# Optimization experiments

Measured on AMD Instinct MI355X. Metric: run time of the kernel, lower is better.

Reference implementation:

```python
import jax, jax.numpy as jnp
import numpy as np

V, C, L, NH, NKV, HID, E, K, T, B = 32000, 1536, 2, 12, 4, 2048, 8, 2, 2048, 1
D = C // NH  # 128
NREP = NH // NKV
EPS = 1e-6

def _rms(x, w):
    return x * jax.lax.rsqrt(jnp.mean(x * x, axis=-1, keepdims=True) + EPS) * w


def setup_inputs() -> dict:
    key = jax.random.key(0)
    ks = jax.random.split(key, 14)
    s = 0.02
    inp = {
        "tokens": jax.random.randint(ks[0], (B, T), 0, V, dtype=jnp.int64),
        "emb": jax.random.normal(ks[1], (V, C), jnp.float32) * s,      # tied with output proj
        "pos": jax.random.normal(ks[2], (T, C), jnp.float32) * s,
        "wq": jax.random.normal(ks[3], (L, C, NH * D), jnp.float32) * s,
        "wk": jax.random.normal(ks[4], (L, C, NKV * D), jnp.float32) * s,
        "wv": jax.random.normal(ks[5], (L, C, NKV * D), jnp.float32) * s,
        "wo": jax.random.normal(ks[6], (L, C, C), jnp.float32) * s,
        "attn_norm_w": jnp.ones((L, C), jnp.float32),
        "ffn_norm_w": jnp.ones((L, C), jnp.float32),
        "gate": jax.random.normal(ks[7], (L, C, E), jnp.float32) * s,
        "ew1": jax.random.normal(ks[8], (L, E, C, HID), jnp.float32) * s,
        "ew2": jax.random.normal(ks[9], (L, E, HID, C), jnp.float32) * s,
        "ew3": jax.random.normal(ks[10], (L, E, C, HID), jnp.float32) * s,
        "final_norm_w": jnp.ones((C,), jnp.float32),
    }
    return inp


def _forward(tokens, emb, pos, wq, wk, wv, wo, attn_norm_w, ffn_norm_w, gate,
             ew1, ew2, ew3, final_norm_w):
    x = emb[tokens] + pos[None, :T]            # [B,T,C]; dropout=0 (eval)
    causal = jnp.tril(jnp.ones((T, T), bool))
    for l in range(L):
        # --- GQA attention ---
        h = _rms(x, attn_norm_w[l])
        q = (h @ wq[l]).reshape(B, T, NH, D).transpose(0, 2, 1, 3)     # [B,NH,T,D]
        k = (h @ wk[l]).reshape(B, T, NKV, D).transpose(0, 2, 1, 3)
        v = (h @ wv[l]).reshape(B, T, NKV, D).transpose(0, 2, 1, 3)
        k = jnp.repeat(k, NREP, axis=1)
        v = jnp.repeat(v, NREP, axis=1)
        scores = jnp.einsum("bhqd,bhkd->bhqk", q, k) / jnp.sqrt(jnp.float32(D))
        scores = jnp.where(causal, scores, jnp.finfo(scores.dtype).min)
        attn = jax.nn.softmax(scores, axis=-1)
        y = jnp.einsum("bhqk,bhkd->bhqd", attn, v)
        y = y.transpose(0, 2, 1, 3).reshape(B, T, C)
        x = x + y @ wo[l]
        # --- MoE FFN (top-k routed SwiGLU experts) ---
        xf = _rms(x, ffn_norm_w[l]).reshape(-1, C)                      # [N,C]
        probs = jax.nn.softmax(xf @ gate[l], axis=-1)                   # [N,E]
        topw, topi = jax.lax.top_k(probs, K)
        topw = topw / jnp.sum(topw, axis=-1, keepdims=True)
        dense_w = jnp.sum(jax.nn.one_hot(topi, E, dtype=xf.dtype) * topw[..., None], axis=1)  # [N,E]
        h1 = jnp.einsum("nc,ech->enh", xf, ew1[l])
        h3 = jnp.einsum("nc,ech->enh", xf, ew3[l])
        hh = jax.nn.silu(h1) * h3                                       # [E,N,HID]
        moe = jnp.einsum("ne,enh,ehc->nc", dense_w, hh, ew2[l])
        x = x + moe.reshape(B, T, C)
    x = _rms(x, final_norm_w)
    logits = x @ emb.T                                                   # tied output proj
    return logits


def reference(tokens, emb, pos, wq, wk, wv, wo, attn_norm_w, ffn_norm_w, gate,
              ew1, ew2, ew3, final_norm_w):
    return _forward(tokens, emb, pos, wq, wk, wv, wo, attn_norm_w, ffn_norm_w,
                    gate, ew1, ew2, ew3, final_norm_w)
```

## Files before the change

kernel.cpp:

```cpp
#include <hip/hip_runtime.h>
#include <hip/hip_bf16.h>
#include <math.h>

#define Tn   2048
#define Cn   1536
#define Vn   32000
#define NHn  12
#define NKVn 4
#define Dn   128
#define HIDn 2048
#define En   8
#define Kn   2
#define Ln   2
#define NREPn 3
#define EPSn 1e-6f

using bf16 = __hip_bfloat16;
using bf16x8 = __attribute__((ext_vector_type(8))) short;
using f32x4v = __attribute__((ext_vector_type(4))) float;

__device__ __forceinline__ void split3(float v, short& h, short& m, short& lo) {
  bf16 b0 = __float2bfloat16(v);
  float r1 = v - __bfloat162float(b0);
  bf16 b1 = __float2bfloat16(r1);
  float r2 = r1 - __bfloat162float(b1);
  bf16 b2 = __float2bfloat16(r2);
  h = *reinterpret_cast<short*>(&b0);
  m = *reinterpret_cast<short*>(&b1);
  lo = *reinterpret_cast<short*>(&b2);
}
__device__ __forceinline__ float b2f(short s) {
  bf16 b = *reinterpret_cast<bf16*>(&s);
  return __bfloat162float(b);
}
__device__ __forceinline__ void gl_lds16(const void* g, void* l) {
  __builtin_amdgcn_global_load_lds((const __attribute__((address_space(1))) void*)g,
                                   (__attribute__((address_space(3))) void*)l, 16, 0, 0);
}

__global__ void embed_k(const int* __restrict__ tok, const float* __restrict__ emb,
                        const float* __restrict__ pos, float* __restrict__ x) {
  int n = blockIdx.x;
  int t = threadIdx.x;
  int id = tok[n];
  const float* er = emb + (size_t)id * Cn;
  const float* pr = pos + (size_t)n * Cn;
  float* xr = x + (size_t)n * Cn;
  for (int c = t; c < Cn; c += 256) xr[c] = er[c] + pr[c];
}

__global__ void rmsnorm_k(const float* __restrict__ x, const float* __restrict__ w,
                          float* __restrict__ out) {
  int n = blockIdx.x, t = threadIdx.x;
  const float* xr = x + (size_t)n * Cn;
  float v[6];
  float ss = 0.f;
#pragma unroll
  for (int i = 0; i < 6; i++) { v[i] = xr[t + i * 256]; ss += v[i] * v[i]; }
  for (int off = 32; off > 0; off >>= 1) ss += __shfl_down(ss, off, 64);
  __shared__ float red[4];
  __shared__ float rtot;
  int wave = t >> 6, lane = t & 63;
  if (lane == 0) red[wave] = ss;
  __syncthreads();
  if (t == 0) rtot = rsqrtf((red[0] + red[1] + red[2] + red[3]) / (float)Cn + EPSn);
  __syncthreads();
  float r = rtot;
  float* orow = out + (size_t)n * Cn;
#pragma unroll
  for (int i = 0; i < 6; i++) { int c = t + i * 256; orow[c] = v[i] * r * w[c]; }
}

__global__ void f2b_k(const float* __restrict__ s, bf16* __restrict__ d, size_t n4) {
  size_t i = (size_t)blockIdx.x * 256 + threadIdx.x;
  size_t stride = (size_t)gridDim.x * 256;
  for (; i < n4; i += stride) {
    float4 v = ((const float4*)s)[i];
    d[i * 4 + 0] = __float2bfloat16(v.x);
    d[i * 4 + 1] = __float2bfloat16(v.y);
    d[i * 4 + 2] = __float2bfloat16(v.z);
    d[i * 4 + 3] = __float2bfloat16(v.w);
  }
}

__global__ void splita_k(const float* __restrict__ s, short* __restrict__ dh,
                         short* __restrict__ dm, short* __restrict__ dl, size_t n4) {
  size_t i = (size_t)blockIdx.x * 256 + threadIdx.x;
  size_t stride = (size_t)gridDim.x * 256;
  for (; i < n4; i += stride) {
    float4 v = ((const float4*)s)[i];
    float a[4] = {v.x, v.y, v.z, v.w};
#pragma unroll
    for (int u = 0; u < 4; u++) {
      short h, m, lo;
      split3(a[u], h, m, lo);
      dh[i * 4 + u] = h; dm[i * 4 + u] = m; dl[i * 4 + u] = lo;
    }
  }
}

__global__ void transp3_k(const float* __restrict__ src, short* __restrict__ dh,
                          short* __restrict__ dm, short* __restrict__ dl, int K, int N) {
  __shared__ __align__(16) float ls[32][33];
  size_t boff = (size_t)blockIdx.z * K * N;
  int k0 = blockIdx.x * 32, n0 = blockIdx.y * 32;
  int t = threadIdx.x;
  int kr = t >> 3, n4 = (t & 7) * 4;
  float4 vv = *(const float4*)&src[boff + (size_t)(k0 + kr) * N + n0 + n4];
  ls[kr][n4 + 0] = vv.x; ls[kr][n4 + 1] = vv.y; ls[kr][n4 + 2] = vv.z; ls[kr][n4 + 3] = vv.w;
  __syncthreads();
  int nr = t >> 3, k4 = (t & 7) * 4;
  size_t dbase = boff + (size_t)(n0 + nr) * K + k0 + k4;
#pragma unroll
  for (int u = 0; u < 4; u++) {
    short h, m, lo;
    split3(ls[k4 + u][nr], h, m, lo);
    dh[dbase + u] = h; dm[dbase + u] = m; dl[dbase + u] = lo;
  }
}

__global__ void transp_k(const float* __restrict__ src, bf16* __restrict__ dst, int K, int N) {
  __shared__ __align__(16) float ls[32][33];
  size_t boff = (size_t)blockIdx.z * K * N;
  int k0 = blockIdx.x * 32, n0 = blockIdx.y * 32;
  int t = threadIdx.x;
  int kr = t >> 3, n4 = (t & 7) * 4;
  float4 vv = *(const float4*)&src[boff + (size_t)(k0 + kr) * N + n0 + n4];
  ls[kr][n4 + 0] = vv.x; ls[kr][n4 + 1] = vv.y; ls[kr][n4 + 2] = vv.z; ls[kr][n4 + 3] = vv.w;
  __syncthreads();
  int nr = t >> 3, k4 = (t & 7) * 4;
  bf16* drow = dst + boff + (size_t)(n0 + nr) * K + k0 + k4;
#pragma unroll
  for (int u = 0; u < 4; u++) drow[u] = __float2bfloat16(ls[k4 + u][nr]);
}

__global__ void __launch_bounds__(256) gemm_btl(const bf16* __restrict__ A, const bf16* __restrict__ Bt,
                                                const float* res, float* Co, int M, int N, int K) {
  __shared__ __align__(16) bf16 As[128 * 32];
  __shared__ __align__(16) bf16 Bs[128 * 32];
  int t = threadIdx.x;
  int l = t & 63, w = t >> 6;
  int bm = blockIdx.x * 128, bn = blockIdx.y * 128;
  int wr = (w >> 1) * 64, wc = (w & 1) * 64;
  const f32x4v zero = {0.f, 0.f, 0.f, 0.f};
  f32x4v acc[4][4];
#pragma unroll
  for (int i = 0; i < 4; i++)
#pragma unroll
    for (int j = 0; j < 4; j++) acc[i][j] = zero;
  const bf16* ag0 = A + (size_t)(bm + (t >> 2)) * K + (t & 3) * 8;
  const bf16* ag1 = A + (size_t)(bm + 64 + (t >> 2)) * K + (t & 3) * 8;
  const bf16* bg0 = Bt + (size_t)(bn + (t >> 2)) * K + (t & 3) * 8;
  const bf16* bg1 = Bt + (size_t)(bn + 64 + (t >> 2)) * K + (t & 3) * 8;
  int rl = l & 15, ko = (l >> 4) * 8;
  for (int k0 = 0; k0 < K; k0 += 32) {
    gl_lds16(ag0 + k0, (char*)As + t * 16);
    gl_lds16(ag1 + k0, (char*)As + (256 + t) * 16);
    gl_lds16(bg0 + k0, (char*)Bs + t * 16);
    gl_lds16(bg1 + k0, (char*)Bs + (256 + t) * 16);
    __syncthreads();
    bf16x8 a[4], b[4];
#pragma unroll
    for (int i = 0; i < 4; i++) a[i] = *(const bf16x8*)(As + (wr + i * 16 + rl) * 32 + ko);
#pragma unroll
    for (int j = 0; j < 4; j++) b[j] = *(const bf16x8*)(Bs + (wc + j * 16 + rl) * 32 + ko);
#pragma unroll
    for (int i = 0; i < 4; i++)
#pragma unroll
      for (int j = 0; j < 4; j++)
        acc[i][j] = __builtin_amdgcn_mfma_f32_16x16x32_bf16(a[i], b[j], acc[i][j], 0, 0, 0);
    __syncthreads();
  }
#pragma unroll
  for (int i = 0; i < 4; i++) {
    int rbase = bm + wr + i * 16 + (l >> 4) * 4;
#pragma unroll
    for (int j = 0; j < 4; j++) {
      int col = bn + wc + j * 16 + (l & 15);
#pragma unroll
      for (int r = 0; r < 4; r++) {
        size_t idx = (size_t)(rbase + r) * N + col;
        float v = acc[i][j][r];
        if (res) v += res[idx];
        Co[idx] = v;
      }
    }
  }
}

__global__ void __launch_bounds__(256) gemm6(const bf16* __restrict__ AH, const bf16* __restrict__ AM,
                                             const bf16* __restrict__ AL,
                                             const bf16* __restrict__ BH, const bf16* __restrict__ BM,
                                             const bf16* __restrict__ BL,
                                             const float* res, float* __restrict__ Co,
                                             int M, int N, int K) {
  __shared__ __align__(16) bf16 sAH[128 * 32], sAM[128 * 32], sAL[128 * 32];
  __shared__ __align__(16) bf16 sBH[128 * 32], sBM[128 * 32], sBL[128 * 32];
  int t = threadIdx.x;
  int l = t & 63, w = t >> 6;
  int bm = blockIdx.x * 128, bn = blockIdx.y * 128;
  int wr = (w >> 1) * 64, wc = (w & 1) * 64;
  const f32x4v zero = {0.f, 0.f, 0.f, 0.f};
  f32x4v acc[4][4];
#pragma unroll
  for (int i = 0; i < 4; i++)
#pragma unroll
    for (int j = 0; j < 4; j++) acc[i][j] = zero;
  size_t a0 = (size_t)(bm + (t >> 2)) * K + (t & 3) * 8;
  size_t a1 = (size_t)(bm + 64 + (t >> 2)) * K + (t & 3) * 8;
  size_t b0 = (size_t)(bn + (t >> 2)) * K + (t & 3) * 8;
  size_t b1 = (size_t)(bn + 64 + (t >> 2)) * K + (t & 3) * 8;
  int rl = l & 15, ko = (l >> 4) * 8;
  for (int k0 = 0; k0 < K; k0 += 32) {
    gl_lds16(AH + a0 + k0, (char*)sAH + t * 16);
    gl_lds16(AH + a1 + k0, (char*)sAH + (256 + t) * 16);
    gl_lds16(AM + a0 + k0, (char*)sAM + t * 16);
    gl_lds16(AM + a1 + k0, (char*)sAM + (256 + t) * 16);
    gl_lds16(AL + a0 + k0, (char*)sAL + t * 16);
    gl_lds16(AL + a1 + k0, (char*)sAL + (256 + t) * 16);
    gl_lds16(BH + b0 + k0, (char*)sBH + t * 16);
    gl_lds16(BH + b1 + k0, (char*)sBH + (256 + t) * 16);
    gl_lds16(BM + b0 + k0, (char*)sBM + t * 16);
    gl_lds16(BM + b1 + k0, (char*)sBM + (256 + t) * 16);
    gl_lds16(BL + b0 + k0, (char*)sBL + t * 16);
    gl_lds16(BL + b1 + k0, (char*)sBL + (256 + t) * 16);
    __syncthreads();
    bf16x8 aH[4], aM[4], aL[4];
#pragma unroll
    for (int i = 0; i < 4; i++) {
      int ro = (wr + i * 16 + rl) * 32 + ko;
      aH[i] = *(const bf16x8*)(sAH + ro);
      aM[i] = *(const bf16x8*)(sAM + ro);
      aL[i] = *(const bf16x8*)(sAL + ro);
    }
#pragma unroll
    for (int j = 0; j < 4; j++) {
      int ro = (wc + j * 16 + rl) * 32 + ko;
      bf16x8 bh = *(const bf16x8*)(sBH + ro);
      bf16x8 bm_ = *(const bf16x8*)(sBM + ro);
      bf16x8 bl = *(const bf16x8*)(sBL + ro);
#pragma unroll
      for (int i = 0; i < 4; i++) {
        acc[i][j] = __builtin_amdgcn_mfma_f32_16x16x32_bf16(aL[i], bh, acc[i][j], 0, 0, 0);
        acc[i][j] = __builtin_amdgcn_mfma_f32_16x16x32_bf16(aH[i], bl, acc[i][j], 0, 0, 0);
        acc[i][j] = __builtin_amdgcn_mfma_f32_16x16x32_bf16(aM[i], bm_, acc[i][j], 0, 0, 0);
        acc[i][j] = __builtin_amdgcn_mfma_f32_16x16x32_bf16(aM[i], bh, acc[i][j], 0, 0, 0);
        acc[i][j] = __builtin_amdgcn_mfma_f32_16x16x32_bf16(aH[i], bm_, acc[i][j], 0, 0, 0);
        acc[i][j] = __builtin_amdgcn_mfma_f32_16x16x32_bf16(aH[i], bh, acc[i][j], 0, 0, 0);
      }
    }
    __syncthreads();
  }
#pragma unroll
  for (int i = 0; i < 4; i++) {
    int rbase = bm + wr + i * 16 + (l >> 4) * 4;
#pragma unroll
    for (int j = 0; j < 4; j++) {
      int col = bn + wc + j * 16 + (l & 15);
#pragma unroll
      for (int r = 0; r < 4; r++) {
        size_t idx = (size_t)(rbase + r) * N + col;
        float v = acc[i][j][r];
        if (res) v += res[idx];
        Co[idx] = v;
      }
    }
  }
}

__global__ void __launch_bounds__(256) mexp6(const bf16* __restrict__ AH, const bf16* __restrict__ AM,
                                             const bf16* __restrict__ AL,
                                             const bf16* __restrict__ BH, const bf16* __restrict__ BM,
                                             const bf16* __restrict__ BL,
                                             const int* __restrict__ perm, const int* __restrict__ cnt,
                                             int ebase,
                                             short* __restrict__ HH, short* __restrict__ HM,
                                             short* __restrict__ HL,
                                             float* __restrict__ Co, int K, int N, int mode) {
  int e = ebase + blockIdx.z;
  int nrows = cnt[e];
  int bm = blockIdx.x * 128;
  if (bm >= nrows) return;
  int bn = blockIdx.y * 128;
  size_t eoff = (size_t)blockIdx.z * K * N;
  __shared__ __align__(16) bf16 sAH[128 * 32], sAM[128 * 32], sAL[128 * 32];
  __shared__ __align__(16) bf16 sBH[128 * 32], sBM[128 * 32], sBL[128 * 32];
  __shared__ int prow[128];
  int t = threadIdx.x, l = t & 63, w = t >> 6;
  if (t < 128) {
    int i = bm + t;
    prow[t] = (i < nrows) ? perm[e * Tn + i] : -1;
  }
  __syncthreads();
  int wr = (w >> 1) * 64, wc = (w & 1) * 64;
  const f32x4v zero = {0.f, 0.f, 0.f, 0.f};
  f32x4v acc[4][4];
#pragma unroll
  for (int i = 0; i < 4; i++)
#pragma unroll
    for (int j = 0; j < 4; j++) acc[i][j] = zero;
  int p0 = prow[t >> 2], p1 = prow[64 + (t >> 2)];
  int g0r = (p0 >= 0) ? (mode == 2 ? p0 : (p0 >> 1)) : 0;
  int g1r = (p1 >= 0) ? (mode == 2 ? p1 : (p1 >> 1)) : 0;
  size_t a0 = (size_t)g0r * K + (t & 3) * 8;
  size_t a1 = (size_t)g1r * K + (t & 3) * 8;
  size_t b0 = eoff + (size_t)(bn + (t >> 2)) * K + (t & 3) * 8;
  size_t b1 = eoff + (size_t)(bn + 64 + (t >> 2)) * K + (t & 3) * 8;
  int rl = l & 15, ko = (l >> 4) * 8;
  for (int k0 = 0; k0 < K; k0 += 32) {
    gl_lds16(AH + a0 + k0, (char*)sAH + t * 16);
    gl_lds16(AH + a1 + k0, (char*)sAH + (256 + t) * 16);
    gl_lds16(AM + a0 + k0, (char*)sAM + t * 16);
    gl_lds16(AM + a1 + k0, (char*)sAM + (256 + t) * 16);
    gl_lds16(AL + a0 + k0, (char*)sAL + t * 16);
    gl_lds16(AL + a1 + k0, (char*)sAL + (256 + t) * 16);
    gl_lds16(BH + b0 + k0, (char*)sBH + t * 16);
    gl_lds16(BH + b1 + k0, (char*)sBH + (256 + t) * 16);
    gl_lds16(BM + b0 + k0, (char*)sBM + t * 16);
    gl_lds16(BM + b1 + k0, (char*)sBM + (256 + t) * 16);
    gl_lds16(BL + b0 + k0, (char*)sBL + t * 16);
    gl_lds16(BL + b1 + k0, (char*)sBL + (256 + t) * 16);
    __syncthreads();
    bf16x8 aH[4], aM[4], aL[4];
#pragma unroll
    for (int i = 0; i < 4; i++) {
      int ro = (wr + i * 16 + rl) * 32 + ko;
      aH[i] = *(const bf16x8*)(sAH + ro);
      aM[i] = *(const bf16x8*)(sAM + ro);
      aL[i] = *(const bf16x8*)(sAL + ro);
    }
#pragma unroll
    for (int j = 0; j < 4; j++) {
      int ro = (wc + j * 16 + rl) * 32 + ko;
      bf16x8 bh = *(const bf16x8*)(sBH + ro);
      bf16x8 bm_ = *(const bf16x8*)(sBM + ro);
      bf16x8 bl = *(const bf16x8*)(sBL + ro);
#pragma unroll
      for (int i = 0; i < 4; i++) {
        acc[i][j] = __builtin_amdgcn_mfma_f32_16x16x32_bf16(aL[i], bh, acc[i][j], 0, 0, 0);
        acc[i][j] = __builtin_amdgcn_mfma_f32_16x16x32_bf16(aH[i], bl, acc[i][j], 0, 0, 0);
        acc[i][j] = __builtin_amdgcn_mfma_f32_16x16x32_bf16(aM[i], bm_, acc[i][j], 0, 0, 0);
        acc[i][j] = __builtin_amdgcn_mfma_f32_16x16x32_bf16(aM[i], bh, acc[i][j], 0, 0, 0);
        acc[i][j] = __builtin_amdgcn_mfma_f32_16x16x32_bf16(aH[i], bm_, acc[i][j], 0, 0, 0);
        acc[i][j] = __builtin_amdgcn_mfma_f32_16x16x32_bf16(aH[i], bh, acc[i][j], 0, 0, 0);
      }
    }
    __syncthreads();
  }
#pragma unroll
  for (int i = 0; i < 4; i++) {
#pragma unroll
    for (int r = 0; r < 4; r++) {
      int lrow = wr + i * 16 + (l >> 4) * 4 + r;
      int p = prow[lrow];
      if (p < 0) continue;
#pragma unroll
      for (int j = 0; j < 4; j++) {
        int col = bn + wc + j * 16 + (l & 15);
        size_t idx = (size_t)p * N + col;
        float v = acc[i][j][r];
        if (mode == 0) {
          short h, m, lo;
          split3(v, h, m, lo);
          HH[idx] = h; HM[idx] = m; HL[idx] = lo;
        } else if (mode == 1) {
          float v1 = b2f(HH[idx]) + b2f(HM[idx]) + b2f(HL[idx]);
          float hh = (v1 / (1.f + expf(-v1))) * v;
          short h, m, lo;
          split3(hh, h, m, lo);
          HH[idx] = h; HM[idx] = m; HL[idx] = lo;
        } else {
          Co[idx] = v;
        }
      }
    }
  }
}

__global__ void __launch_bounds__(256) mexpB(const bf16* __restrict__ A, const bf16* __restrict__ B,
                                             const int* __restrict__ perm, const int* __restrict__ cnt,
                                             int ebase, bf16* __restrict__ HB,
                                             float* __restrict__ Co, int K, int N, int mode) {
  int e = ebase + blockIdx.z;
  int nrows = cnt[e];
  int bm = blockIdx.x * 128;
  if (bm >= nrows) return;
  int bn = blockIdx.y * 128;
  size_t eoff = (size_t)blockIdx.z * K * N;
  __shared__ __align__(16) bf16 sA[128 * 32];
  __shared__ __align__(16) bf16 sB[128 * 32];
  __shared__ int prow[128];
  int t = threadIdx.x, l = t & 63, w = t >> 6;
  if (t < 128) {
    int i = bm + t;
    prow[t] = (i < nrows) ? perm[e * Tn + i] : -1;
  }
  __syncthreads();
  int wr = (w >> 1) * 64, wc = (w & 1) * 64;
  const f32x4v zero = {0.f, 0.f, 0.f, 0.f};
  f32x4v acc[4][4];
#pragma unroll
  for (int i = 0; i < 4; i++)
#pragma unroll
    for (int j = 0; j < 4; j++) acc[i][j] = zero;
  int p0 = prow[t >> 2], p1 = prow[64 + (t >> 2)];
  int g0r = (p0 >= 0) ? (mode == 2 ? p0 : (p0 >> 1)) : 0;
  int g1r = (p1 >= 0) ? (mode == 2 ? p1 : (p1 >> 1)) : 0;
  size_t a0 = (size_t)g0r * K + (t & 3) * 8;
  size_t a1 = (size_t)g1r * K + (t & 3) * 8;
  size_t b0 = eoff + (size_t)(bn + (t >> 2)) * K + (t & 3) * 8;
  size_t b1 = eoff + (size_t)(bn + 64 + (t >> 2)) * K + (t & 3) * 8;
  int rl = l & 15, ko = (l >> 4) * 8;
  for (int k0 = 0; k0 < K; k0 += 32) {
    gl_lds16(A + a0 + k0, (char*)sA + t * 16);
    gl_lds16(A + a1 + k0, (char*)sA + (256 + t) * 16);
    gl_lds16(B + b0 + k0, (char*)sB + t * 16);
    gl_lds16(B + b1 + k0, (char*)sB + (256 + t) * 16);
    __syncthreads();
    bf16x8 a[4], b[4];
#pragma unroll
    for (int i = 0; i < 4; i++) a[i] = *(const bf16x8*)(sA + (wr + i * 16 + rl) * 32 + ko);
#pragma unroll
    for (int j = 0; j < 4; j++) b[j] = *(const bf16x8*)(sB + (wc + j * 16 + rl) * 32 + ko);
#pragma unroll
    for (int i = 0; i < 4; i++)
#pragma unroll
      for (int j = 0; j < 4; j++)
        acc[i][j] = __builtin_amdgcn_mfma_f32_16x16x32_bf16(a[i], b[j], acc[i][j], 0, 0, 0);
    __syncthreads();
  }
#pragma unroll
  for (int i = 0; i < 4; i++) {
#pragma unroll
    for (int r = 0; r < 4; r++) {
      int lrow = wr + i * 16 + (l >> 4) * 4 + r;
      int p = prow[lrow];
      if (p < 0) continue;
#pragma unroll
      for (int j = 0; j < 4; j++) {
        int col = bn + wc + j * 16 + (l & 15);
        size_t idx = (size_t)p * N + col;
        float v = acc[i][j][r];
        if (mode == 0) {
          HB[idx] = __float2bfloat16(v);
        } else if (mode == 1) {
          float v1 = __bfloat162float(HB[idx]);
          HB[idx] = __float2bfloat16((v1 / (1.f + expf(-v1))) * v);
        } else {
          Co[idx] = v;
        }
      }
    }
  }
}

__global__ void __launch_bounds__(256) attn_fast_k(const float* __restrict__ q,
                                                   const float* __restrict__ k,
                                                   const float* __restrict__ v,
                                                   float* __restrict__ y) {
  int qt = gridDim.x - 1 - blockIdx.x;
  int head = blockIdx.y;
  int kvh = head / NREPn;
  int q0 = qt * 32;
  int t = threadIdx.x;
  int r = t >> 3, g = t & 7, d0 = g * 16;
  __shared__ __align__(16) float ks[32][Dn + 4];
  __shared__ __align__(16) float vs[32][Dn + 4];
  const float scale = 0.08838834764831845f;
  float qr[16];
  {
    const float* qrow = q + (size_t)(q0 + r) * (NHn * Dn) + head * Dn + d0;
#pragma unroll
    for (int j = 0; j < 16; j += 4) {
      float4 u = *(const float4*)(qrow + j);
      qr[j] = u.x * scale; qr[j + 1] = u.y * scale;
      qr[j + 2] = u.z * scale; qr[j + 3] = u.w * scale;
    }
  }
  float o[16];
#pragma unroll
  for (int j = 0; j < 16; j++) o[j] = 0.f;
  float rowm = -1e30f, rowl = 0.f;

  for (int kt = 0; kt <= qt; kt++) {
    int kv0 = kt * 32;
    for (int e = t; e < 32 * 32; e += 256) {
      int rr = e >> 5, c4 = (e & 31) * 4;
      size_t off = (size_t)(kv0 + rr) * (NKVn * Dn) + kvh * Dn + c4;
      *(float4*)&ks[rr][c4] = *(const float4*)(k + off);
      *(float4*)&vs[rr][c4] = *(const float4*)(v + off);
    }
    __syncthreads();
    float s[32];
#pragma unroll
    for (int kk = 0; kk < 32; kk++) {
      const float* krow = &ks[kk][d0];
      float p = 0.f;
#pragma unroll
      for (int j = 0; j < 16; j += 4) {
        float4 u = *(const float4*)(krow + j);
        p += qr[j] * u.x + qr[j + 1] * u.y + qr[j + 2] * u.z + qr[j + 3] * u.w;
      }
      p += __shfl_xor(p, 1);
      p += __shfl_xor(p, 2);
      p += __shfl_xor(p, 4);
      s[kk] = p;
    }
    if (kt == qt) {
#pragma unroll
      for (int kk = 0; kk < 32; kk++)
        if (kk > r) s[kk] = -1e30f;
    }
    float mx = s[0];
#pragma unroll
    for (int kk = 1; kk < 32; kk++) mx = fmaxf(mx, s[kk]);
    float m_new = fmaxf(rowm, mx);
    float corr = expf(rowm - m_new);
    float sum = 0.f;
#pragma unroll
    for (int kk = 0; kk < 32; kk++) { s[kk] = expf(s[kk] - m_new); sum += s[kk]; }
    rowl = rowl * corr + sum;
    rowm = m_new;
#pragma unroll
    for (int j = 0; j < 16; j++) o[j] *= corr;
#pragma unroll
    for (int kk = 0; kk < 32; kk++) {
      float p = s[kk];
      const float* vrow = &vs[kk][d0];
#pragma unroll
      for (int j = 0; j < 16; j += 4) {
        float4 u = *(const float4*)(vrow + j);
        o[j] += p * u.x; o[j + 1] += p * u.y; o[j + 2] += p * u.z; o[j + 3] += p * u.w;
      }
    }
    __syncthreads();
  }
  float inv = 1.f / rowl;
  float* yrow = y + (size_t)(q0 + r) * (NHn * Dn) + head * Dn + d0;
#pragma unroll
  for (int j = 0; j < 16; j += 4) {
    float4 u;
    u.x = o[j] * inv; u.y = o[j + 1] * inv; u.z = o[j + 2] * inv; u.w = o[j + 3] * inv;
    *(float4*)(yrow + j) = u;
  }
}

__global__ void gate_k(const float* __restrict__ xf, const float* __restrict__ g,
                       float* __restrict__ gl) {
  int n = blockIdx.x, t = threadIdx.x;
  int e = t & 7, cs = t >> 3;
  const float* xr = xf + (size_t)n * Cn;
  float s = 0.f;
  for (int j = 0; j < Cn / 32; j++) {
    int c = cs + 32 * j;
    s += xr[c] * g[c * En + e];
  }
  __shared__ float red[256];
  red[t] = s;
  __syncthreads();
  if (t < 8) {
    float tot = 0.f;
    for (int j = 0; j < 32; j++) tot += red[t + 8 * j];
    gl[n * En + t] = tot;
  }
}

__global__ void route_k(const float* __restrict__ gl, float* __restrict__ topw,
                        int* __restrict__ cnt, int* __restrict__ perm) {
  int n = blockIdx.x * blockDim.x + threadIdx.x;
  if (n >= Tn) return;
  float p[En];
  float mx = -1e30f;
#pragma unroll
  for (int e = 0; e < En; e++) { p[e] = gl[n * En + e]; mx = fmaxf(mx, p[e]); }
  float s = 0.f;
#pragma unroll
  for (int e = 0; e < En; e++) { p[e] = expf(p[e] - mx); s += p[e]; }
  float invs = 1.f / s;
#pragma unroll
  for (int e = 0; e < En; e++) p[e] *= invs;
  int i0 = 0;
#pragma unroll
  for (int e = 1; e < En; e++) if (p[e] > p[i0]) i0 = e;
  int i1 = (i0 == 0) ? 1 : 0;
#pragma unroll
  for (int e = 0; e < En; e++) if (e != i0 && p[e] > p[i1]) i1 = e;
  float w0 = p[i0], w1 = p[i1], sw = w0 + w1;
  topw[2 * n]     = w0 / sw;
  topw[2 * n + 1] = w1 / sw;
  int pos0 = atomicAdd(&cnt[i0], 1);
  perm[i0 * Tn + pos0] = 2 * n;
  int pos1 = atomicAdd(&cnt[i1], 1);
  perm[i1 * Tn + pos1] = 2 * n + 1;
}

__global__ void combine_k(const float* __restrict__ pairout, const float* __restrict__ topw,
                          float* __restrict__ x) {
  int n = blockIdx.x, t = threadIdx.x;
  float w0 = topw[2 * n], w1 = topw[2 * n + 1];
  const float* p0 = pairout + (size_t)(2 * n) * Cn;
  const float* p1 = pairout + (size_t)(2 * n + 1) * Cn;
  float* xr = x + (size_t)n * Cn;
  for (int c = t; c < Cn; c += 256) xr[c] += w0 * p0[c] + w1 * p1[c];
}

extern "C" void kernel_launch(void* const* d_in, const int* in_sizes, int n_in,
                              void* d_out, int out_size, void* d_ws, size_t ws_size,
                              hipStream_t stream) {
  const int*   tokens = (const int*)d_in[0];
  const float* emb    = (const float*)d_in[1];
  const float* pos    = (const float*)d_in[2];
  const float* wq     = (const float*)d_in[3];
  const float* wk     = (const float*)d_in[4];
  const float* wv     = (const float*)d_in[5];
  const float* wo     = (const float*)d_in[6];
  const float* attn_nw= (const float*)d_in[7];
  const float* ffn_nw = (const float*)d_in[8];
  const float* gate   = (const float*)d_in[9];
  const float* ew1    = (const float*)d_in[10];
  const float* ew2    = (const float*)d_in[11];
  const float* ew3    = (const float*)d_in[12];
  const float* final_nw = (const float*)d_in[13];
  float* out = (float*)d_out;

  char* wsb = (char*)d_ws;
  const size_t NC = (size_t)Tn * Cn;
  size_t off = 0;
  auto alloc = [&](size_t bytes) -> size_t {
    off = (off + 255) & ~(size_t)255;
    size_t p = off;
    off += bytes;
    return p;
  };
  size_t o_x    = alloc(NC * 4);
  size_t o_h    = alloc(NC * 4);
  size_t o_gl   = alloc((size_t)Tn * En * 4);
  size_t o_topw = alloc((size_t)Tn * Kn * 4);
  size_t o_cnt  = alloc(64);
  size_t o_perm = alloc((size_t)En * Tn * 4);
  size_t wlvl   = (size_t)4 * Cn * HIDn * 2;
  size_t o_w    = alloc(3 * wlvl);
  size_t hs_lvl = NC * 2;
  size_t o_hs   = alloc(3 * hs_lvl);
  size_t o_qb   = alloc(NC * 4);
  size_t o_kb   = alloc((size_t)Tn * NKVn * Dn * 4);
  size_t o_vb   = alloc((size_t)Tn * NKVn * Dn * 4);
  size_t o_yb   = alloc(NC * 4);
  size_t hb_lvl = (size_t)Tn * Kn * HIDn * 2;
  size_t o_hbs  = o_qb;
  size_t end_hbs = o_hbs + 3 * hb_lvl;
  if (off < end_hbs) off = end_hbs;
  size_t o_pair = alloc(NC * 4);

  float* x       = (float*)(wsb + o_x);
  float* h       = (float*)(wsb + o_h);
  float* gl      = (float*)(wsb + o_gl);
  float* topw    = (float*)(wsb + o_topw);
  int*   cnt     = (int*)(wsb + o_cnt);
  int*   perm    = (int*)(wsb + o_perm);
  float* qb      = (float*)(wsb + o_qb);
  float* kb      = (float*)(wsb + o_kb);
  float* vb      = (float*)(wsb + o_vb);
  float* yb      = (float*)(wsb + o_yb);
  float* pairout = (float*)(wsb + o_pair);
  bf16*  hb      = (bf16*)(wsb + o_pair);
  bf16*  embB    = (bf16*)(wsb + o_w);

  short* hs[3]; short* hbs[3]; short* ewT[3];
  for (int s = 0; s < 3; s++) {
    hs[s]  = (short*)(wsb + o_hs + (size_t)s * hs_lvl);
    hbs[s] = (short*)(wsb + o_hbs + (size_t)s * hb_lvl);
    ewT[s] = (short*)(wsb + o_w + (size_t)s * wlvl);
  }
  size_t wq_lvl = (size_t)Cn * (NHn * Dn) * 2;
  size_t wk_lvl = (size_t)Cn * (NKVn * Dn) * 2;
  short* wqT[3]; short* wkT[3]; short* wvT[3]; short* woT[3];
  {
    size_t p = o_w;
    for (int s = 0; s < 3; s++) { wqT[s] = (short*)(wsb + p); p += wq_lvl; }
    for (int s = 0; s < 3; s++) { wkT[s] = (short*)(wsb + p); p += wk_lvl; }
    for (int s = 0; s < 3; s++) { wvT[s] = (short*)(wsb + p); p += wk_lvl; }
    for (int s = 0; s < 3; s++) { woT[s] = (short*)(wsb + p); p += wq_lvl; }
  }

  embed_k<<<Tn, 256, 0, stream>>>(tokens, emb, pos, x);
  for (int l = 0; l < Ln; l++) {
    const float* wq_l = wq + (size_t)l * Cn * (NHn * Dn);
    const float* wk_l = wk + (size_t)l * Cn * (NKVn * Dn);
    const float* wv_l = wv + (size_t)l * Cn * (NKVn * Dn);
    const float* wo_l = wo + (size_t)l * Cn * Cn;
    const float* g_l  = gate + (size_t)l * Cn * En;
    const float* e1_l = ew1 + (size_t)l * En * Cn * HIDn;
    const float* e2_l = ew2 + (size_t)l * En * HIDn * Cn;
    const float* e3_l = ew3 + (size_t)l * En * Cn * HIDn;

    transp3_k<<<dim3(Cn / 32, (NHn * Dn) / 32, 1), 256, 0, stream>>>(wq_l, wqT[0], wqT[1], wqT[2], Cn, NHn * Dn);
    transp3_k<<<dim3(Cn / 32, (NKVn * Dn) / 32, 1), 256, 0, stream>>>(wk_l, wkT[0], wkT[1], wkT[2], Cn, NKVn * Dn);
    transp3_k<<<dim3(Cn / 32, (NKVn * Dn) / 32, 1), 256, 0, stream>>>(wv_l, wvT[0], wvT[1], wvT[2], Cn, NKVn * Dn);
    transp3_k<<<dim3(Cn / 32, Cn / 32, 1), 256, 0, stream>>>(wo_l, woT[0], woT[1], woT[2], Cn, Cn);
    rmsnorm_k<<<Tn, 256, 0, stream>>>(x, attn_nw + (size_t)l * Cn, h);
    splita_k<<<2048, 256, 0, stream>>>(h, hs[0], hs[1], hs[2], NC / 4);
    gemm6<<<dim3(Tn / 128, (NHn * Dn) / 128), 256, 0, stream>>>(
        (bf16*)hs[0], (bf16*)hs[1], (bf16*)hs[2], (bf16*)wqT[0], (bf16*)wqT[1], (bf16*)wqT[2],
        nullptr, qb, Tn, NHn * Dn, Cn);
    gemm6<<<dim3(Tn / 128, (NKVn * Dn) / 128), 256, 0, stream>>>(
        (bf16*)hs[0], (bf16*)hs[1], (bf16*)hs[2], (bf16*)wkT[0], (bf16*)wkT[1], (bf16*)wkT[2],
        nullptr, kb, Tn, NKVn * Dn, Cn);
    gemm6<<<dim3(Tn / 128, (NKVn * Dn) / 128), 256, 0, stream>>>(
        (bf16*)hs[0], (bf16*)hs[1], (bf16*)hs[2], (bf16*)wvT[0], (bf16*)wvT[1], (bf16*)wvT[2],
        nullptr, vb, Tn, NKVn * Dn, Cn);
    attn_fast_k<<<dim3(Tn / 32, NHn), 256, 0, stream>>>(qb, kb, vb, yb);
    splita_k<<<2048, 256, 0, stream>>>(yb, hs[0], hs[1], hs[2], NC / 4);
    gemm6<<<dim3(Tn / 128, Cn / 128), 256, 0, stream>>>(
        (bf16*)hs[0], (bf16*)hs[1], (bf16*)hs[2], (bf16*)woT[0], (bf16*)woT[1], (bf16*)woT[2],
        x, x, Tn, Cn, Cn);

    rmsnorm_k<<<Tn, 256, 0, stream>>>(x, ffn_nw + (size_t)l * Cn, h);
    gate_k<<<Tn, 256, 0, stream>>>(h, g_l, gl);
    hipMemsetAsync(cnt, 0, 64, stream);
    route_k<<<Tn / 256, 256, 0, stream>>>(gl, topw, cnt, perm);

    if (l < Ln - 1) {
      splita_k<<<2048, 256, 0, stream>>>(h, hs[0], hs[1], hs[2], NC / 4);
      for (int half = 0; half < 2; half++) {
        size_t hoff = (size_t)half * 4 * Cn * HIDn;
        int eb = half * 4;
        transp3_k<<<dim3(Cn / 32, HIDn / 32, 4), 256, 0, stream>>>(e1_l + hoff, ewT[0], ewT[1], ewT[2], Cn, HIDn);
        mexp6<<<dim3(Tn / 128, HIDn / 128, 4), 256, 0, stream>>>(
            (bf16*)hs[0], (bf16*)hs[1], (bf16*)hs[2], (bf16*)ewT[0], (bf16*)ewT[1], (bf16*)ewT[2],
            perm, cnt, eb, hbs[0], hbs[1], hbs[2], nullptr, Cn, HIDn, 0);
        transp3_k<<<dim3(Cn / 32, HIDn / 32, 4), 256, 0, stream>>>(e3_l + hoff, ewT[0], ewT[1], ewT[2], Cn, HIDn);
        mexp6<<<dim3(Tn / 128, HIDn / 128, 4), 256, 0, stream>>>(
            (bf16*)hs[0], (bf16*)hs[1], (bf16*)hs[2], (bf16*)ewT[0], (bf16*)ewT[1], (bf16*)ewT[2],
            perm, cnt, eb, hbs[0], hbs[1], hbs[2], nullptr, Cn, HIDn, 1);
        transp3_k<<<dim3(HIDn / 32, Cn / 32, 4), 256, 0, stream>>>(e2_l + hoff, ewT[0], ewT[1], ewT[2], HIDn, Cn);
        mexp6<<<dim3(Tn / 128, Cn / 128, 4), 256, 0, stream>>>(
            (bf16*)hbs[0], (bf16*)hbs[1], (bf16*)hbs[2], (bf16*)ewT[0], (bf16*)ewT[1], (bf16*)ewT[2],
            perm, cnt, eb, hbs[0], hbs[1], hbs[2], pairout, HIDn, Cn, 2);
      }
    } else {
      f2b_k<<<2048, 256, 0, stream>>>(h, (bf16*)hs[0], NC / 4);
      for (int half = 0; half < 2; half++) {
        size_t hoff = (size_t)half * 4 * Cn * HIDn;
        int eb = half * 4;
        transp_k<<<dim3(Cn / 32, HIDn / 32, 4), 256, 0, stream>>>(e1_l + hoff, (bf16*)ewT[0], Cn, HIDn);
        mexpB<<<dim3(Tn / 128, HIDn / 128, 4), 256, 0, stream>>>(
            (bf16*)hs[0], (bf16*)ewT[0], perm, cnt, eb, (bf16*)hbs[0], nullptr, Cn, HIDn, 0);
        transp_k<<<dim3(Cn / 32, HIDn / 32, 4), 256, 0, stream>>>(e3_l + hoff, (bf16*)ewT[0], Cn, HIDn);
        mexpB<<<dim3(Tn / 128, HIDn / 128, 4), 256, 0, stream>>>(
            (bf16*)hs[0], (bf16*)ewT[0], perm, cnt, eb, (bf16*)hbs[0], nullptr, Cn, HIDn, 1);
        transp_k<<<dim3(HIDn / 32, Cn / 32, 4), 256, 0, stream>>>(e2_l + hoff, (bf16*)ewT[0], HIDn, Cn);
        mexpB<<<dim3(Tn / 128, Cn / 128, 4), 256, 0, stream>>>(
            (bf16*)hbs[0], (bf16*)ewT[0], perm, cnt, eb, (bf16*)hbs[0], pairout, HIDn, Cn, 2);
      }
    }
    combine_k<<<Tn, 256, 0, stream>>>(pairout, topw, x);
  }
  rmsnorm_k<<<Tn, 256, 0, stream>>>(x, final_nw, h);
  f2b_k<<<2048, 256, 0, stream>>>(h, hb, NC / 4);
  f2b_k<<<2048, 256, 0, stream>>>(emb, embB, (size_t)Vn * Cn / 4);
  gemm_btl<<<dim3(Tn / 128, Vn / 128), 256, 0, stream>>>(hb, embB, nullptr, out, Tn, Vn, Cn);
}
```

Before: 5.780 ms.

## Split causal attention over KV chunks with a separate merge kernel

The attention kernel now splits each query tile's KV range into chunks of 16 tiles across a third grid dimension, so up to four blocks work on one query tile. Each block writes an unnormalized partial output with its running max and sum, and a new merge kernel combines them log-sum-exp style. The goal is to shorten the critical path of late query tiles and improve load balance and occupancy with only 12 heads. The cost is extra global traffic for partials, an extra launch, and idle early-exit blocks.

```diff
diff --git a/kernel.cpp b/kernel.cpp
--- a/kernel.cpp
+++ b/kernel.cpp
@@ -14,6 +14,8 @@
 #define Ln   2
 #define NREPn 3
 #define EPSn 1e-6f
+#define CHT  16
+#define NCHn 4
 
 using bf16 = __hip_bfloat16;
 using bf16x8 = __attribute__((ext_vector_type(8))) short;
@@ -454,22 +456,30 @@
   }
 }
 
-__global__ void __launch_bounds__(256) attn_fast_k(const float* __restrict__ q,
+__global__ void __launch_bounds__(256) attn_part_k(const float* __restrict__ q,
                                                    const float* __restrict__ k,
                                                    const float* __restrict__ v,
-                                                   float* __restrict__ y) {
-  int qt = gridDim.x - 1 - blockIdx.x;
+                                                   float* __restrict__ po,
+                                                   float* __restrict__ pm,
+                                                   float* __restrict__ pl) {
+  int qt = blockIdx.x;
   int head = blockIdx.y;
+  int ch = blockIdx.z;
+  int ntiles = qt + 1;
+  int tA = ch * CHT;
+  if (tA >= ntiles) return;
+  int tB = tA + CHT < ntiles ? tA + CHT : ntiles;
   int kvh = head / NREPn;
   int q0 = qt * 32;
   int t = threadIdx.x;
   int r = t >> 3, g = t & 7, d0 = g * 16;
+  int row = q0 + r;
   __shared__ __align__(16) float ks[32][Dn + 4];
   __shared__ __align__(16) float vs[32][Dn + 4];
   const float scale = 0.08838834764831845f;
   float qr[16];
   {
-    const float* qrow = q + (size_t)(q0 + r) * (NHn * Dn) + head * Dn + d0;
+    const float* qrow = q + (size_t)row * (NHn * Dn) + head * Dn + d0;
 #pragma unroll
     for (int j = 0; j < 16; j += 4) {
       float4 u = *(const float4*)(qrow + j);
@@ -482,7 +492,7 @@
   for (int j = 0; j < 16; j++) o[j] = 0.f;
   float rowm = -1e30f, rowl = 0.f;
 
-  for (int kt = 0; kt <= qt; kt++) {
+  for (int kt = tA; kt < tB; kt++) {
     int kv0 = kt * 32;
     for (int e = t; e < 32 * 32; e += 256) {
       int rr = e >> 5, c4 = (e & 31) * 4;
@@ -535,12 +545,53 @@
     }
     __syncthreads();
   }
-  float inv = 1.f / rowl;
-  float* yrow = y + (size_t)(q0 + r) * (NHn * Dn) + head * Dn + d0;
+  size_t pidx = ((size_t)head * Tn + row) * NCHn + ch;
+  if (g == 0) { pm[pidx] = rowm; pl[pidx] = rowl; }
+  float* porow = po + pidx * Dn + d0;
 #pragma unroll
   for (int j = 0; j < 16; j += 4) {
     float4 u;
-    u.x = o[j] * inv; u.y = o[j + 1] * inv; u.z = o[j + 2] * inv; u.w = o[j + 3] * inv;
+    u.x = o[j]; u.y = o[j + 1]; u.z = o[j + 2]; u.w = o[j + 3];
+    *(float4*)(porow + j) = u;
+  }
+}
+
+__global__ void __launch_bounds__(256) attn_merge_k(const float* __restrict__ po,
+                                                    const float* __restrict__ pm,
+                                                    const float* __restrict__ pl,
+                                                    float* __restrict__ y) {
+  int qt = blockIdx.x;
+  int head = blockIdx.y;
+  int q0 = qt * 32;
+  int t = threadIdx.x;
+  int r = t >> 3, g = t & 7, d0 = g * 16;
+  int row = q0 + r;
+  int nach = (qt + CHT) / CHT;
+  size_t base = ((size_t)head * Tn + row) * NCHn;
+  float M = -1e30f;
+  for (int c = 0; c < nach; c++) M = fmaxf(M, pm[base + c]);
+  float L = 0.f;
+  float acc[16];
+#pragma unroll
+  for (int j = 0; j < 16; j++) acc[j] = 0.f;
+  for (int c = 0; c < nach; c++) {
+    float wgt = expf(pm[base + c] - M);
+    L += pl[base + c] * wgt;
+    const float* p = po + (base + c) * Dn + d0;
+#pragma unroll
+    for (int j = 0; j < 16; j += 4) {
+      float4 u = *(const float4*)(p + j);
+      acc[j] += wgt * u.x; acc[j + 1] += wgt * u.y;
+      acc[j + 2] += wgt * u.z; acc[j + 3] += wgt * u.w;
+    }
+  }
+  float inv = 1.f / L;
+  float* yrow = y + (size_t)row * (NHn * Dn) + head * Dn + d0;
+#pragma unroll
+  for (int j = 0; j < 16; j += 4) {
+    float4 u;
+    u.x = acc[j] * inv; u.y = acc[j + 1] * inv;
+    u.z = acc[j + 2] * inv; u.w = acc[j + 3] * inv;
     *(float4*)(yrow + j) = u;
   }
 }
@@ -651,6 +702,9 @@
   size_t end_hbs = o_hbs + 3 * hb_lvl;
   if (off < end_hbs) off = end_hbs;
   size_t o_pair = alloc(NC * 4);
+  size_t o_po   = alloc((size_t)NHn * Tn * NCHn * Dn * 4);
+  size_t o_pm   = alloc((size_t)NHn * Tn * NCHn * 4);
+  size_t o_pl   = alloc((size_t)NHn * Tn * NCHn * 4);
 
   float* x       = (float*)(wsb + o_x);
   float* h       = (float*)(wsb + o_h);
@@ -665,6 +719,9 @@
   float* pairout = (float*)(wsb + o_pair);
   bf16*  hb      = (bf16*)(wsb + o_pair);
   bf16*  embB    = (bf16*)(wsb + o_w);
+  float* po      = (float*)(wsb + o_po);
+  float* pm      = (float*)(wsb + o_pm);
+  float* pl      = (float*)(wsb + o_pl);
 
   short* hs[3]; short* hbs[3]; short* ewT[3];
   for (int s = 0; s < 3; s++) {
@@ -709,7 +766,8 @@
     gemm6<<<dim3(Tn / 128, (NKVn * Dn) / 128), 256, 0, stream>>>(
         (bf16*)hs[0], (bf16*)hs[1], (bf16*)hs[2], (bf16*)wvT[0], (bf16*)wvT[1], (bf16*)wvT[2],
         nullptr, vb, Tn, NKVn * Dn, Cn);
-    attn_fast_k<<<dim3(Tn / 32, NHn), 256, 0, stream>>>(qb, kb, vb, yb);
+    attn_part_k<<<dim3(Tn / 32, NHn, NCHn), 256, 0, stream>>>(qb, kb, vb, po, pm, pl);
+    attn_merge_k<<<dim3(Tn / 32, NHn), 256, 0, stream>>>(po, pm, pl, yb);
     splita_k<<<2048, 256, 0, stream>>>(yb, hs[0], hs[1], hs[2], NC / 4);
     gemm6<<<dim3(Tn / 128, Cn / 128), 256, 0, stream>>>(
         (bf16*)hs[0], (bf16*)hs[1], (bf16*)hs[2], (bf16*)woT[0], (bf16*)woT[1], (bf16*)woT[2],
```

After: 5.301 ms. 8.3% less time.
